# Performance work log

Hardware: AMD Instinct MI355X
Metric: run time of the kernel (lower is better)

The kernel has to match this reference:

```python
import jax, jax.numpy as jnp
import numpy as np

HEADS = 16
DIM_HEAD = 64
RMS_EPS = 1.1920929e-07  # torch.finfo(float32).eps (torch RMSNorm eps=None default)
ROPE_THETA = 10000.0


def _rope(x):
    # x: [b, h, n, d]; rotary-embedding-torch style interleaved rotation
    n, d = x.shape[-2], x.shape[-1]
    inv_freq = 1.0 / (ROPE_THETA ** (jnp.arange(0, d, 2, dtype=jnp.float32) / d))
    t = jnp.arange(n, dtype=jnp.float32)
    freqs = t[:, None] * inv_freq[None, :]              # [n, d/2]
    cos = jnp.repeat(jnp.cos(freqs), 2, axis=-1)        # [n, d] interleaved
    sin = jnp.repeat(jnp.sin(freqs), 2, axis=-1)
    x1 = x[..., ::2]
    x2 = x[..., 1::2]
    rot = jnp.stack((-x2, x1), axis=-1).reshape(x.shape)  # rotate_half, interleaved pairs
    return x * cos + rot * sin


def setup_inputs() -> dict:
    key = jax.random.key(0)
    ks = jax.random.split(key, 6)
    b, n, dim = 2, 2048, 1024
    tokens = jax.random.normal(ks[0], (b, n, dim), dtype=jnp.float32)
    norm_weight = jnp.ones((dim,), dtype=jnp.float32)
    wq = jax.random.normal(ks[1], (dim, dim), dtype=jnp.float32) * 0.02
    wk = jax.random.normal(ks[2], (dim, dim), dtype=jnp.float32) * 0.02
    wv = jax.random.normal(ks[3], (dim, dim), dtype=jnp.float32) * 0.02
    wo = jax.random.normal(ks[4], (dim, dim), dtype=jnp.float32) * 0.02
    return {"tokens": tokens, "norm_weight": norm_weight, "wq": wq, "wk": wk, "wv": wv, "wo": wo}


def reference(tokens, norm_weight, wq, wk, wv, wo):
    b, n, dim = tokens.shape
    # RMSNorm (elementwise affine)
    x = tokens * jax.lax.rsqrt(jnp.mean(tokens * tokens, axis=-1, keepdims=True) + RMS_EPS)
    x = x * norm_weight
    # QKV projections (torch Linear: x @ W.T), split heads: b n (h d) -> b h n d
    def split(y):
        return y.reshape(b, n, HEADS, DIM_HEAD).transpose(0, 2, 1, 3)
    q = split(x @ wq.T) * (DIM_HEAD ** -0.5)
    k = split(x @ wk.T)
    v = split(x @ wv.T)
    # rotary embedding (no kv cache -> same positions for q and k)
    q = _rope(q)
    k = _rope(k)
    sim = jnp.einsum('bhid,bhjd->bhij', q, k)
    causal = jnp.triu(jnp.ones((n, n), dtype=bool), k=1)
    sim = jnp.where(causal, -jnp.finfo(sim.dtype).max, sim)
    attn = jax.nn.softmax(sim, axis=-1)
    out = jnp.einsum('bhij,bhjd->bhid', attn, v)
    out = out.transpose(0, 2, 1, 3).reshape(b, n, dim)  # merge heads
    return out @ wo.T
```

## Files before the change

kernel.cpp:

```cpp
#include <hip/hip_runtime.h>

typedef __bf16 bf16x8 __attribute__((ext_vector_type(8)));
typedef float f32x4 __attribute__((ext_vector_type(4)));

#define DIM 1024
#define NSEQ 2048

#define GL2LDS(g, l) __builtin_amdgcn_global_load_lds( \
    (const __attribute__((address_space(1))) void*)(g), \
    (__attribute__((address_space(3))) void*)(l), 16, 0, 0)

__global__ __launch_bounds__(256) void cvt_kernel(const float* __restrict__ s,
                                                  __bf16* __restrict__ d) {
    int i = (blockIdx.x * 256 + threadIdx.x) * 4;
    float4 f = *(const float4*)(s + i);
    union { uint2 u; __bf16 h[4]; } p;
    p.h[0] = (__bf16)f.x; p.h[1] = (__bf16)f.y;
    p.h[2] = (__bf16)f.z; p.h[3] = (__bf16)f.w;
    *(uint2*)(d + i) = p.u;
}

__global__ __launch_bounds__(256) void rmsnorm_kernel(const float* __restrict__ x,
                                                      const float* __restrict__ g,
                                                      __bf16* __restrict__ o) {
    int row = blockIdx.x;
    int t = threadIdx.x;
    float4 xv = ((const float4*)(x + (size_t)row * DIM))[t];
    float ss = xv.x*xv.x + xv.y*xv.y + xv.z*xv.z + xv.w*xv.w;
    #pragma unroll
    for (int off = 32; off; off >>= 1) ss += __shfl_xor(ss, off, 64);
    __shared__ float red[4];
    if ((t & 63) == 0) red[t >> 6] = ss;
    __syncthreads();
    ss = red[0] + red[1] + red[2] + red[3];
    float r = rsqrtf(ss * (1.0f / 1024.0f) + 1.1920929e-07f);
    float4 gv = ((const float4*)g)[t];
    union { uint2 u; __bf16 h[4]; } p;
    p.h[0] = (__bf16)(xv.x * r * gv.x);
    p.h[1] = (__bf16)(xv.y * r * gv.y);
    p.h[2] = (__bf16)(xv.z * r * gv.z);
    p.h[3] = (__bf16)(xv.w * r * gv.w);
    *(uint2*)(o + (size_t)row * DIM + t * 4) = p.u;
}

__global__ __launch_bounds__(256) void rope_kernel(__bf16* __restrict__ x) {
    int gid = blockIdx.x * 256 + threadIdx.x;
    int row = gid >> 9;
    int pr = gid & 511;
    int pos = row & (NSEQ - 1);
    int dp = pr & 31;
    float inv = __expf(-(float)dp * (9.210340371976184f / 32.0f));
    float ang = (float)pos * inv;
    float sn, cs;
    sincosf(ang, &sn, &cs);
    size_t off = (size_t)row * DIM + pr * 2;
    union { unsigned int u; __bf16 h[2]; } p;
    p.u = *(const unsigned int*)(x + off);
    float x1 = (float)p.h[0], x2 = (float)p.h[1];
    p.h[0] = (__bf16)(x1 * cs - x2 * sn);
    p.h[1] = (__bf16)(x2 * cs + x1 * sn);
    *(unsigned int*)(x + off) = p.u;
}

template <typename CT>
__device__ __forceinline__ void gemm_body(const __bf16* __restrict__ A,
                                          const __bf16* __restrict__ B,
                                          CT* __restrict__ C,
                                          int mb, int nb, int ldc, float scale,
                                          __bf16* As, __bf16* Bs) {
    int t = threadIdx.x;
    int w = t >> 6, l = t & 63;
    int wm = (w >> 1) * 64, wn = (w & 1) * 64;
    int lrow = l & 15, lq = l >> 4;
    f32x4 acc[4][4] = {};

    int srow = w * 16 + (l >> 2);
    int sc8 = (l & 3) * 8;
    const __bf16* gA = A + (size_t)(mb * 128 + srow) * 1024 + sc8;
    const __bf16* gB = B + (size_t)(nb * 128 + srow) * 1024 + sc8;
    __bf16* lA = As + (w * 64) * 8;
    __bf16* lB = Bs + (w * 64) * 8;

    for (int kt = 0; kt < 32; ++kt) {
        int k0 = kt * 32;
        GL2LDS(gA + k0, lA);
        GL2LDS(gA + k0 + (size_t)64 * 1024, lA + 256 * 8);
        GL2LDS(gB + k0, lB);
        GL2LDS(gB + k0 + (size_t)64 * 1024, lB + 256 * 8);
        __syncthreads();
        bf16x8 af[4], bfr[4];
        #pragma unroll
        for (int i = 0; i < 4; ++i)
            af[i] = *(const bf16x8*)&As[(wm + i * 16 + lrow) * 32 + lq * 8];
        #pragma unroll
        for (int i = 0; i < 4; ++i)
            bfr[i] = *(const bf16x8*)&Bs[(wn + i * 16 + lrow) * 32 + lq * 8];
        #pragma unroll
        for (int rt = 0; rt < 4; ++rt)
            #pragma unroll
            for (int ct = 0; ct < 4; ++ct)
                acc[rt][ct] = __builtin_amdgcn_mfma_f32_16x16x32_bf16(
                    af[rt], bfr[ct], acc[rt][ct], 0, 0, 0);
        __syncthreads();
    }
    #pragma unroll
    for (int rt = 0; rt < 4; ++rt)
        #pragma unroll
        for (int ct = 0; ct < 4; ++ct)
            #pragma unroll
            for (int r = 0; r < 4; ++r) {
                int row = mb * 128 + wm + rt * 16 + lq * 4 + r;
                int col = nb * 128 + wn + ct * 16 + lrow;
                C[(size_t)row * ldc + col] = (CT)(acc[rt][ct][r] * scale);
            }
}

__global__ __launch_bounds__(256) void qkv_kernel(const __bf16* __restrict__ x,
                                                  const __bf16* __restrict__ wq,
                                                  const __bf16* __restrict__ wk,
                                                  const __bf16* __restrict__ wv,
                                                  __bf16* __restrict__ qb,
                                                  __bf16* __restrict__ kb,
                                                  __bf16* __restrict__ vtb) {
    __shared__ __bf16 As[128 * 32];
    __shared__ __bf16 Bs[128 * 32];
    int bm = blockIdx.x, bn = blockIdx.y, z = blockIdx.z;
    if (z == 0)      gemm_body<__bf16>(x,  wq, qb,  bm, bn, 1024, 0.125f, As, Bs);
    else if (z == 1) gemm_body<__bf16>(x,  wk, kb,  bm, bn, 1024, 1.0f,   As, Bs);
    else             gemm_body<__bf16>(wv, x,  vtb, bn, bm, 4096, 1.0f,   As, Bs);
}

__global__ __launch_bounds__(256) void wo_kernel(const __bf16* __restrict__ A,
                                                 const __bf16* __restrict__ B,
                                                 float* __restrict__ C) {
    __shared__ __bf16 As[128 * 32];
    __shared__ __bf16 Bs[128 * 32];
    gemm_body<float>(A, B, C, blockIdx.x, blockIdx.y, 1024, 1.0f, As, Bs);
}

__global__ __launch_bounds__(256, 4) void attn_kernel(const __bf16* __restrict__ q,
                                                      const __bf16* __restrict__ kk,
                                                      const __bf16* __restrict__ vt,
                                                      __bf16* __restrict__ o) {
    int blk = blockIdx.x;
    int qt = 31 - (blk & 31);
    int h = (blk >> 5) & 15;
    int b = blk >> 9;
    int rowbase = b * NSEQ;
    int t = threadIdx.x;
    int w = t >> 6, l = t & 63;
    int lrow = l & 15, lq = l >> 4;

    __shared__ __bf16 Kt[64 * 72];
    __shared__ __bf16 Vs[64 * 72];
    __shared__ __bf16 Ps[4 * 16 * 72];
    __bf16* pw = &Ps[w * 16 * 72];

    const __bf16* kbase = kk + (size_t)rowbase * DIM + h * 64;
    const __bf16* vbase = vt + (size_t)(h * 64) * 4096 + b * 2048;

    int row0 = t >> 3;
    int c8 = (t & 7) * 8;

    const __bf16* qp = q + (size_t)(rowbase + qt * 64 + w * 16 + lrow) * DIM + h * 64;
    bf16x8 qb0 = *(const bf16x8*)(qp + lq * 8);
    bf16x8 qb1 = *(const bf16x8*)(qp + 32 + lq * 8);

    f32x4 oacc[4] = {};
    float m_r = -1e30f, l_r = 0.0f;

    uint4 kr0, kr1, vr0, vr1;
    kr0 = *(const uint4*)(kbase + (size_t)row0 * DIM + c8);
    kr1 = *(const uint4*)(kbase + (size_t)(row0 + 32) * DIM + c8);
    vr0 = *(const uint4*)(vbase + (size_t)row0 * 4096 + c8);
    vr1 = *(const uint4*)(vbase + (size_t)(row0 + 32) * 4096 + c8);
    *(uint4*)&Kt[row0 * 72 + c8] = kr0;
    *(uint4*)&Kt[(row0 + 32) * 72 + c8] = kr1;
    *(uint4*)&Vs[row0 * 72 + c8] = vr0;
    *(uint4*)&Vs[(row0 + 32) * 72 + c8] = vr1;
    __syncthreads();

    for (int jt = 0; jt <= qt; ++jt) {
        if (jt < qt) {
            int j0 = (jt + 1) * 64;
            kr0 = *(const uint4*)(kbase + (size_t)(j0 + row0) * DIM + c8);
            kr1 = *(const uint4*)(kbase + (size_t)(j0 + row0 + 32) * DIM + c8);
            vr0 = *(const uint4*)(vbase + (size_t)row0 * 4096 + j0 + c8);
            vr1 = *(const uint4*)(vbase + (size_t)(row0 + 32) * 4096 + j0 + c8);
        }

        f32x4 st[4];
        #pragma unroll
        for (int ct = 0; ct < 4; ++ct) {
            f32x4 z = {};
            bf16x8 ka0 = *(const bf16x8*)&Kt[(ct * 16 + lrow) * 72 + lq * 8];
            bf16x8 ka1 = *(const bf16x8*)&Kt[(ct * 16 + lrow) * 72 + 32 + lq * 8];
            z = __builtin_amdgcn_mfma_f32_16x16x32_bf16(ka0, qb0, z, 0, 0, 0);
            z = __builtin_amdgcn_mfma_f32_16x16x32_bf16(ka1, qb1, z, 0, 0, 0);
            st[ct] = z;
        }
        if (jt == qt) {
            int qr = w * 16 + lrow;
            #pragma unroll
            for (int ct = 0; ct < 4; ++ct)
                #pragma unroll
                for (int r = 0; r < 4; ++r)
                    if (ct * 16 + lq * 4 + r > qr) st[ct][r] = -3.0e38f;
        }
        float mx = st[0][0];
        #pragma unroll
        for (int ct = 0; ct < 4; ++ct)
            #pragma unroll
            for (int r = 0; r < 4; ++r) mx = fmaxf(mx, st[ct][r]);
        mx = fmaxf(mx, __shfl_xor(mx, 16, 64));
        mx = fmaxf(mx, __shfl_xor(mx, 32, 64));
        float mnew = fmaxf(m_r, mx);
        float alpha = __expf(m_r - mnew);
        float ps = 0.0f;
        #pragma unroll
        for (int ct = 0; ct < 4; ++ct)
            #pragma unroll
            for (int r = 0; r < 4; ++r) {
                float p = __expf(st[ct][r] - mnew);
                st[ct][r] = p;
                ps += p;
            }
        ps += __shfl_xor(ps, 16, 64);
        ps += __shfl_xor(ps, 32, 64);
        l_r = l_r * alpha + ps;
        m_r = mnew;

        #pragma unroll
        for (int ct = 0; ct < 4; ++ct) {
            union { uint2 u; __bf16 h4[4]; } pk;
            #pragma unroll
            for (int r = 0; r < 4; ++r) pk.h4[r] = (__bf16)st[ct][r];
            *(uint2*)&pw[lrow * 72 + ct * 16 + lq * 4] = pk.u;
        }
        #pragma unroll
        for (int ct = 0; ct < 4; ++ct)
            #pragma unroll
            for (int r = 0; r < 4; ++r) oacc[ct][r] *= alpha;
        bf16x8 pb0 = *(const bf16x8*)&pw[lrow * 72 + lq * 8];
        bf16x8 pb1 = *(const bf16x8*)&pw[lrow * 72 + 32 + lq * 8];
        #pragma unroll
        for (int ct = 0; ct < 4; ++ct) {
            bf16x8 va0 = *(const bf16x8*)&Vs[(ct * 16 + lrow) * 72 + lq * 8];
            bf16x8 va1 = *(const bf16x8*)&Vs[(ct * 16 + lrow) * 72 + 32 + lq * 8];
            oacc[ct] = __builtin_amdgcn_mfma_f32_16x16x32_bf16(va0, pb0, oacc[ct], 0, 0, 0);
            oacc[ct] = __builtin_amdgcn_mfma_f32_16x16x32_bf16(va1, pb1, oacc[ct], 0, 0, 0);
        }
        __syncthreads();
        if (jt < qt) {
            *(uint4*)&Kt[row0 * 72 + c8] = kr0;
            *(uint4*)&Kt[(row0 + 32) * 72 + c8] = kr1;
            *(uint4*)&Vs[row0 * 72 + c8] = vr0;
            *(uint4*)&Vs[(row0 + 32) * 72 + c8] = vr1;
        }
        __syncthreads();
    }
    float rcp = 1.0f / l_r;
    const size_t orow = (size_t)(rowbase + qt * 64 + w * 16 + lrow) * DIM + h * 64;
    #pragma unroll
    for (int ct = 0; ct < 4; ++ct) {
        union { uint2 u; __bf16 h4[4]; } pk;
        #pragma unroll
        for (int r = 0; r < 4; ++r) pk.h4[r] = (__bf16)(oacc[ct][r] * rcp);
        *(uint2*)(o + orow + ct * 16 + lq * 4) = pk.u;
    }
}

extern "C" void kernel_launch(void* const* d_in, const int* in_sizes, int n_in,
                              void* d_out, int out_size, void* d_ws, size_t ws_size,
                              hipStream_t stream) {
    const float* tokens = (const float*)d_in[0];
    const float* gamma  = (const float*)d_in[1];
    const float* wq = (const float*)d_in[2];
    const float* wk = (const float*)d_in[3];
    const float* wv = (const float*)d_in[4];
    const float* wo = (const float*)d_in[5];

    __bf16* ws  = (__bf16*)d_ws;
    __bf16* x   = ws;
    __bf16* qb  = x   + (size_t)4096 * 1024;
    __bf16* kb  = qb  + (size_t)4096 * 1024;
    __bf16* vtb = kb  + (size_t)4096 * 1024;
    __bf16* ao  = x;
    __bf16* wob = qb;
    float*  out = (float*)d_out;

    __bf16* wqb = (__bf16*)d_out;
    __bf16* wkb = wqb + (size_t)1024 * 1024;
    __bf16* wvb = wkb + (size_t)1024 * 1024;

    cvt_kernel<<<1024, 256, 0, stream>>>(wq, wqb);
    cvt_kernel<<<1024, 256, 0, stream>>>(wk, wkb);
    cvt_kernel<<<1024, 256, 0, stream>>>(wv, wvb);

    rmsnorm_kernel<<<4096, 256, 0, stream>>>(tokens, gamma, x);

    qkv_kernel<<<dim3(32, 8, 3), 256, 0, stream>>>(x, wqb, wkb, wvb, qb, kb, vtb);

    rope_kernel<<<8192, 256, 0, stream>>>(qb);
    rope_kernel<<<8192, 256, 0, stream>>>(kb);

    attn_kernel<<<1024, 256, 0, stream>>>(qb, kb, vtb, ao);

    cvt_kernel<<<1024, 256, 0, stream>>>(wo, wob);

    wo_kernel<<<dim3(32, 8), 256, 0, stream>>>(ao, wob, out);
}
```

Measured before the change: 224.6 us.

## Enlarge attention Q tile to 128 rows and map blocks per XCD

Each attention block now processes 128 query rows (32 per wave, as two 16-row groups) instead of 64, so every K/V tile loaded into LDS feeds twice as many MFMAs and global K/V traffic is halved. Block IDs are remapped so that blocks for the same batch-head land on the same XCD, which should improve L2 reuse of K/V. Waves whose rows lie entirely before the current KV tile skip compute on the diagonal tiles. The grid halves to 512 blocks and launch bounds drop to 3 waves per SIMD, trading occupancy and parallelism for reuse, with more register pressure.

```diff
diff --git a/kernel.cpp b/kernel.cpp
--- a/kernel.cpp
+++ b/kernel.cpp
@@ -138,14 +138,18 @@
     gemm_body<float>(A, B, C, blockIdx.x, blockIdx.y, 1024, 1.0f, As, Bs);
 }
 
-__global__ __launch_bounds__(256, 4) void attn_kernel(const __bf16* __restrict__ q,
+__global__ __launch_bounds__(256, 3) void attn_kernel(const __bf16* __restrict__ q,
                                                       const __bf16* __restrict__ kk,
                                                       const __bf16* __restrict__ vt,
                                                       __bf16* __restrict__ o) {
-    int blk = blockIdx.x;
-    int qt = 31 - (blk & 31);
-    int h = (blk >> 5) & 15;
-    int b = blk >> 9;
+    int id = blockIdx.x;
+    int xcd = id & 7;
+    int slot = id >> 3;
+    int qt = 15 - (slot >> 2);
+    int bh = xcd * 4 + (slot & 3);
+    int h = bh & 15;
+    int b = bh >> 4;
+    int Q0 = qt * 128;
     int rowbase = b * NSEQ;
     int t = threadIdx.x;
     int w = t >> 6, l = t & 63;
@@ -153,8 +157,8 @@
 
     __shared__ __bf16 Kt[64 * 72];
     __shared__ __bf16 Vs[64 * 72];
-    __shared__ __bf16 Ps[4 * 16 * 72];
-    __bf16* pw = &Ps[w * 16 * 72];
+    __shared__ __bf16 Ps[4 * 32 * 72];
+    __bf16* pw = &Ps[w * 32 * 72];
 
     const __bf16* kbase = kk + (size_t)rowbase * DIM + h * 64;
     const __bf16* vbase = vt + (size_t)(h * 64) * 4096 + b * 2048;
@@ -162,12 +166,14 @@
     int row0 = t >> 3;
     int c8 = (t & 7) * 8;
 
-    const __bf16* qp = q + (size_t)(rowbase + qt * 64 + w * 16 + lrow) * DIM + h * 64;
-    bf16x8 qb0 = *(const bf16x8*)(qp + lq * 8);
-    bf16x8 qb1 = *(const bf16x8*)(qp + 32 + lq * 8);
-
-    f32x4 oacc[4] = {};
-    float m_r = -1e30f, l_r = 0.0f;
+    const __bf16* qp0 = q + (size_t)(rowbase + Q0 + w * 32 + lrow) * DIM + h * 64;
+    bf16x8 qb00 = *(const bf16x8*)(qp0 + lq * 8);
+    bf16x8 qb01 = *(const bf16x8*)(qp0 + 32 + lq * 8);
+    bf16x8 qb10 = *(const bf16x8*)(qp0 + 16 * DIM + lq * 8);
+    bf16x8 qb11 = *(const bf16x8*)(qp0 + 16 * DIM + 32 + lq * 8);
+
+    f32x4 oacc[2][4] = {};
+    float m_r[2] = {-1e30f, -1e30f}, l_r[2] = {0.0f, 0.0f};
 
     uint4 kr0, kr1, vr0, vr1;
     kr0 = *(const uint4*)(kbase + (size_t)row0 * DIM + c8);
@@ -180,78 +186,94 @@
     *(uint4*)&Vs[(row0 + 32) * 72 + c8] = vr1;
     __syncthreads();
 
-    for (int jt = 0; jt <= qt; ++jt) {
-        if (jt < qt) {
-            int j0 = (jt + 1) * 64;
-            kr0 = *(const uint4*)(kbase + (size_t)(j0 + row0) * DIM + c8);
-            kr1 = *(const uint4*)(kbase + (size_t)(j0 + row0 + 32) * DIM + c8);
-            vr0 = *(const uint4*)(vbase + (size_t)row0 * 4096 + j0 + c8);
-            vr1 = *(const uint4*)(vbase + (size_t)(row0 + 32) * 4096 + j0 + c8);
+    int T = 2 * qt + 2;
+    for (int jt = 0; jt < T; ++jt) {
+        int j0 = jt * 64;
+        if (jt + 1 < T) {
+            int jn = j0 + 64;
+            kr0 = *(const uint4*)(kbase + (size_t)(jn + row0) * DIM + c8);
+            kr1 = *(const uint4*)(kbase + (size_t)(jn + row0 + 32) * DIM + c8);
+            vr0 = *(const uint4*)(vbase + (size_t)row0 * 4096 + jn + c8);
+            vr1 = *(const uint4*)(vbase + (size_t)(row0 + 32) * 4096 + jn + c8);
         }
-
-        f32x4 st[4];
-        #pragma unroll
-        for (int ct = 0; ct < 4; ++ct) {
-            f32x4 z = {};
-            bf16x8 ka0 = *(const bf16x8*)&Kt[(ct * 16 + lrow) * 72 + lq * 8];
-            bf16x8 ka1 = *(const bf16x8*)&Kt[(ct * 16 + lrow) * 72 + 32 + lq * 8];
-            z = __builtin_amdgcn_mfma_f32_16x16x32_bf16(ka0, qb0, z, 0, 0, 0);
-            z = __builtin_amdgcn_mfma_f32_16x16x32_bf16(ka1, qb1, z, 0, 0, 0);
-            st[ct] = z;
-        }
-        if (jt == qt) {
-            int qr = w * 16 + lrow;
-            #pragma unroll
-            for (int ct = 0; ct < 4; ++ct)
-                #pragma unroll
-                for (int r = 0; r < 4; ++r)
-                    if (ct * 16 + lq * 4 + r > qr) st[ct][r] = -3.0e38f;
-        }
-        float mx = st[0][0];
-        #pragma unroll
-        for (int ct = 0; ct < 4; ++ct)
-            #pragma unroll
-            for (int r = 0; r < 4; ++r) mx = fmaxf(mx, st[ct][r]);
-        mx = fmaxf(mx, __shfl_xor(mx, 16, 64));
-        mx = fmaxf(mx, __shfl_xor(mx, 32, 64));
-        float mnew = fmaxf(m_r, mx);
-        float alpha = __expf(m_r - mnew);
-        float ps = 0.0f;
-        #pragma unroll
-        for (int ct = 0; ct < 4; ++ct)
-            #pragma unroll
-            for (int r = 0; r < 4; ++r) {
-                float p = __expf(st[ct][r] - mnew);
-                st[ct][r] = p;
-                ps += p;
-            }
-        ps += __shfl_xor(ps, 16, 64);
-        ps += __shfl_xor(ps, 32, 64);
-        l_r = l_r * alpha + ps;
-        m_r = mnew;
-
-        #pragma unroll
-        for (int ct = 0; ct < 4; ++ct) {
-            union { uint2 u; __bf16 h4[4]; } pk;
-            #pragma unroll
-            for (int r = 0; r < 4; ++r) pk.h4[r] = (__bf16)st[ct][r];
-            *(uint2*)&pw[lrow * 72 + ct * 16 + lq * 4] = pk.u;
-        }
-        #pragma unroll
-        for (int ct = 0; ct < 4; ++ct)
-            #pragma unroll
-            for (int r = 0; r < 4; ++r) oacc[ct][r] *= alpha;
-        bf16x8 pb0 = *(const bf16x8*)&pw[lrow * 72 + lq * 8];
-        bf16x8 pb1 = *(const bf16x8*)&pw[lrow * 72 + 32 + lq * 8];
-        #pragma unroll
-        for (int ct = 0; ct < 4; ++ct) {
-            bf16x8 va0 = *(const bf16x8*)&Vs[(ct * 16 + lrow) * 72 + lq * 8];
-            bf16x8 va1 = *(const bf16x8*)&Vs[(ct * 16 + lrow) * 72 + 32 + lq * 8];
-            oacc[ct] = __builtin_amdgcn_mfma_f32_16x16x32_bf16(va0, pb0, oacc[ct], 0, 0, 0);
-            oacc[ct] = __builtin_amdgcn_mfma_f32_16x16x32_bf16(va1, pb1, oacc[ct], 0, 0, 0);
+        bool active = (j0 <= Q0 + w * 32 + 31);
+        if (active) {
+            f32x4 st[2][4];
+            #pragma unroll
+            for (int ct = 0; ct < 4; ++ct) {
+                bf16x8 ka0 = *(const bf16x8*)&Kt[(ct * 16 + lrow) * 72 + lq * 8];
+                bf16x8 ka1 = *(const bf16x8*)&Kt[(ct * 16 + lrow) * 72 + 32 + lq * 8];
+                f32x4 z0 = {}, z1 = {};
+                z0 = __builtin_amdgcn_mfma_f32_16x16x32_bf16(ka0, qb00, z0, 0, 0, 0);
+                z0 = __builtin_amdgcn_mfma_f32_16x16x32_bf16(ka1, qb01, z0, 0, 0, 0);
+                z1 = __builtin_amdgcn_mfma_f32_16x16x32_bf16(ka0, qb10, z1, 0, 0, 0);
+                z1 = __builtin_amdgcn_mfma_f32_16x16x32_bf16(ka1, qb11, z1, 0, 0, 0);
+                st[0][ct] = z0;
+                st[1][ct] = z1;
+            }
+            if (jt >= 2 * qt) {
+                #pragma unroll
+                for (int g = 0; g < 2; ++g) {
+                    int qr = Q0 + w * 32 + g * 16 + lrow;
+                    #pragma unroll
+                    for (int ct = 0; ct < 4; ++ct)
+                        #pragma unroll
+                        for (int r = 0; r < 4; ++r)
+                            if (j0 + ct * 16 + lq * 4 + r > qr) st[g][ct][r] = -3.0e38f;
+                }
+            }
+            #pragma unroll
+            for (int g = 0; g < 2; ++g) {
+                float mx = st[g][0][0];
+                #pragma unroll
+                for (int ct = 0; ct < 4; ++ct)
+                    #pragma unroll
+                    for (int r = 0; r < 4; ++r) mx = fmaxf(mx, st[g][ct][r]);
+                mx = fmaxf(mx, __shfl_xor(mx, 16, 64));
+                mx = fmaxf(mx, __shfl_xor(mx, 32, 64));
+                float mnew = fmaxf(m_r[g], mx);
+                float alpha = __expf(m_r[g] - mnew);
+                float ps = 0.0f;
+                #pragma unroll
+                for (int ct = 0; ct < 4; ++ct)
+                    #pragma unroll
+                    for (int r = 0; r < 4; ++r) {
+                        float p = __expf(st[g][ct][r] - mnew);
+                        st[g][ct][r] = p;
+                        ps += p;
+                    }
+                ps += __shfl_xor(ps, 16, 64);
+                ps += __shfl_xor(ps, 32, 64);
+                l_r[g] = l_r[g] * alpha + ps;
+                m_r[g] = mnew;
+                #pragma unroll
+                for (int ct = 0; ct < 4; ++ct) {
+                    union { uint2 u; __bf16 h4[4]; } pk;
+                    #pragma unroll
+                    for (int r = 0; r < 4; ++r) pk.h4[r] = (__bf16)st[g][ct][r];
+                    *(uint2*)&pw[(g * 16 + lrow) * 72 + ct * 16 + lq * 4] = pk.u;
+                }
+                #pragma unroll
+                for (int ct = 0; ct < 4; ++ct)
+                    #pragma unroll
+                    for (int r = 0; r < 4; ++r) oacc[g][ct][r] *= alpha;
+            }
+            bf16x8 pb00 = *(const bf16x8*)&pw[lrow * 72 + lq * 8];
+            bf16x8 pb01 = *(const bf16x8*)&pw[lrow * 72 + 32 + lq * 8];
+            bf16x8 pb10 = *(const bf16x8*)&pw[(16 + lrow) * 72 + lq * 8];
+            bf16x8 pb11 = *(const bf16x8*)&pw[(16 + lrow) * 72 + 32 + lq * 8];
+            #pragma unroll
+            for (int ct = 0; ct < 4; ++ct) {
+                bf16x8 va0 = *(const bf16x8*)&Vs[(ct * 16 + lrow) * 72 + lq * 8];
+                bf16x8 va1 = *(const bf16x8*)&Vs[(ct * 16 + lrow) * 72 + 32 + lq * 8];
+                oacc[0][ct] = __builtin_amdgcn_mfma_f32_16x16x32_bf16(va0, pb00, oacc[0][ct], 0, 0, 0);
+                oacc[0][ct] = __builtin_amdgcn_mfma_f32_16x16x32_bf16(va1, pb01, oacc[0][ct], 0, 0, 0);
+                oacc[1][ct] = __builtin_amdgcn_mfma_f32_16x16x32_bf16(va0, pb10, oacc[1][ct], 0, 0, 0);
+                oacc[1][ct] = __builtin_amdgcn_mfma_f32_16x16x32_bf16(va1, pb11, oacc[1][ct], 0, 0, 0);
+            }
         }
         __syncthreads();
-        if (jt < qt) {
+        if (jt + 1 < T) {
             *(uint4*)&Kt[row0 * 72 + c8] = kr0;
             *(uint4*)&Kt[(row0 + 32) * 72 + c8] = kr1;
             *(uint4*)&Vs[row0 * 72 + c8] = vr0;
@@ -259,14 +281,17 @@
         }
         __syncthreads();
     }
-    float rcp = 1.0f / l_r;
-    const size_t orow = (size_t)(rowbase + qt * 64 + w * 16 + lrow) * DIM + h * 64;
     #pragma unroll
-    for (int ct = 0; ct < 4; ++ct) {
-        union { uint2 u; __bf16 h4[4]; } pk;
-        #pragma unroll
-        for (int r = 0; r < 4; ++r) pk.h4[r] = (__bf16)(oacc[ct][r] * rcp);
-        *(uint2*)(o + orow + ct * 16 + lq * 4) = pk.u;
+    for (int g = 0; g < 2; ++g) {
+        float rcp = 1.0f / l_r[g];
+        const size_t orow = (size_t)(rowbase + Q0 + w * 32 + g * 16 + lrow) * DIM + h * 64;
+        #pragma unroll
+        for (int ct = 0; ct < 4; ++ct) {
+            union { uint2 u; __bf16 h4[4]; } pk;
+            #pragma unroll
+            for (int r = 0; r < 4; ++r) pk.h4[r] = (__bf16)(oacc[g][ct][r] * rcp);
+            *(uint2*)(o + orow + ct * 16 + lq * 4) = pk.u;
+        }
     }
 }
 
@@ -304,7 +329,7 @@
     rope_kernel<<<8192, 256, 0, stream>>>(qb);
     rope_kernel<<<8192, 256, 0, stream>>>(kb);
 
-    attn_kernel<<<1024, 256, 0, stream>>>(qb, kb, vtb, ao);
+    attn_kernel<<<512, 256, 0, stream>>>(qb, kb, vtb, ao);
 
     cvt_kernel<<<1024, 256, 0, stream>>>(wo, wob);
 
```

New measurement: 215.0 us. -4.3%, faster.

## Use persistent XCD-local attention scheduler, double-buffered K/V, and wider GEMM k-tiles

Applied to the files above, without the earlier changes.

The attention kernel becomes persistent: 512 blocks pull work items from per-XCD atomic counters, longest query tiles first, so load balances across the causal triangle and each XCD keeps to its own heads for L2 locality. K/V tiles are double-buffered in LDS, which removes one barrier per iteration. The GEMM body now loads 64-wide k-tiles with half as many barriers. The costs are more LDS per block, lower occupancy (launch bounds 2), and an extra init kernel whose counters live in the output buffer.

```diff
diff --git a/kernel.cpp b/kernel.cpp
--- a/kernel.cpp
+++ b/kernel.cpp
@@ -19,6 +19,8 @@
     p.h[2] = (__bf16)f.z; p.h[3] = (__bf16)f.w;
     *(uint2*)(d + i) = p.u;
 }
+
+__global__ void init_kernel(int* c) { c[threadIdx.x] = 0; }
 
 __global__ __launch_bounds__(256) void rmsnorm_kernel(const float* __restrict__ x,
                                                       const float* __restrict__ g,
@@ -74,33 +76,37 @@
     int lrow = l & 15, lq = l >> 4;
     f32x4 acc[4][4] = {};
 
-    int srow = w * 16 + (l >> 2);
-    int sc8 = (l & 3) * 8;
+    int srow = w * 32 + (l >> 3);
+    int sc8 = (l & 7) * 8;
     const __bf16* gA = A + (size_t)(mb * 128 + srow) * 1024 + sc8;
     const __bf16* gB = B + (size_t)(nb * 128 + srow) * 1024 + sc8;
-    __bf16* lA = As + (w * 64) * 8;
-    __bf16* lB = Bs + (w * 64) * 8;
-
-    for (int kt = 0; kt < 32; ++kt) {
-        int k0 = kt * 32;
-        GL2LDS(gA + k0, lA);
-        GL2LDS(gA + k0 + (size_t)64 * 1024, lA + 256 * 8);
-        GL2LDS(gB + k0, lB);
-        GL2LDS(gB + k0 + (size_t)64 * 1024, lB + 256 * 8);
+    __bf16* lA = As + (size_t)(w * 32) * 64;
+    __bf16* lB = Bs + (size_t)(w * 32) * 64;
+
+    for (int kt = 0; kt < 16; ++kt) {
+        int k0 = kt * 64;
+        #pragma unroll
+        for (int c = 0; c < 4; ++c) {
+            GL2LDS(gA + (size_t)c * 8 * 1024 + k0, lA + c * 8 * 64);
+            GL2LDS(gB + (size_t)c * 8 * 1024 + k0, lB + c * 8 * 64);
+        }
         __syncthreads();
-        bf16x8 af[4], bfr[4];
         #pragma unroll
-        for (int i = 0; i < 4; ++i)
-            af[i] = *(const bf16x8*)&As[(wm + i * 16 + lrow) * 32 + lq * 8];
-        #pragma unroll
-        for (int i = 0; i < 4; ++i)
-            bfr[i] = *(const bf16x8*)&Bs[(wn + i * 16 + lrow) * 32 + lq * 8];
-        #pragma unroll
-        for (int rt = 0; rt < 4; ++rt)
-            #pragma unroll
-            for (int ct = 0; ct < 4; ++ct)
-                acc[rt][ct] = __builtin_amdgcn_mfma_f32_16x16x32_bf16(
-                    af[rt], bfr[ct], acc[rt][ct], 0, 0, 0);
+        for (int ch = 0; ch < 2; ++ch) {
+            bf16x8 af[4], bfr[4];
+            #pragma unroll
+            for (int i = 0; i < 4; ++i)
+                af[i] = *(const bf16x8*)&As[(wm + i * 16 + lrow) * 64 + ch * 32 + lq * 8];
+            #pragma unroll
+            for (int i = 0; i < 4; ++i)
+                bfr[i] = *(const bf16x8*)&Bs[(wn + i * 16 + lrow) * 64 + ch * 32 + lq * 8];
+            #pragma unroll
+            for (int rt = 0; rt < 4; ++rt)
+                #pragma unroll
+                for (int ct = 0; ct < 4; ++ct)
+                    acc[rt][ct] = __builtin_amdgcn_mfma_f32_16x16x32_bf16(
+                        af[rt], bfr[ct], acc[rt][ct], 0, 0, 0);
+        }
         __syncthreads();
     }
     #pragma unroll
@@ -122,8 +128,8 @@
                                                   __bf16* __restrict__ qb,
                                                   __bf16* __restrict__ kb,
                                                   __bf16* __restrict__ vtb) {
-    __shared__ __bf16 As[128 * 32];
-    __shared__ __bf16 Bs[128 * 32];
+    __shared__ __bf16 As[128 * 64];
+    __shared__ __bf16 Bs[128 * 64];
     int bm = blockIdx.x, bn = blockIdx.y, z = blockIdx.z;
     if (z == 0)      gemm_body<__bf16>(x,  wq, qb,  bm, bn, 1024, 0.125f, As, Bs);
     else if (z == 1) gemm_body<__bf16>(x,  wk, kb,  bm, bn, 1024, 1.0f,   As, Bs);
@@ -133,140 +139,148 @@
 __global__ __launch_bounds__(256) void wo_kernel(const __bf16* __restrict__ A,
                                                  const __bf16* __restrict__ B,
                                                  float* __restrict__ C) {
-    __shared__ __bf16 As[128 * 32];
-    __shared__ __bf16 Bs[128 * 32];
+    __shared__ __bf16 As[128 * 64];
+    __shared__ __bf16 Bs[128 * 64];
     gemm_body<float>(A, B, C, blockIdx.x, blockIdx.y, 1024, 1.0f, As, Bs);
 }
 
-__global__ __launch_bounds__(256, 4) void attn_kernel(const __bf16* __restrict__ q,
+__global__ __launch_bounds__(256, 2) void attn_kernel(const __bf16* __restrict__ q,
                                                       const __bf16* __restrict__ kk,
                                                       const __bf16* __restrict__ vt,
-                                                      __bf16* __restrict__ o) {
-    int blk = blockIdx.x;
-    int qt = 31 - (blk & 31);
-    int h = (blk >> 5) & 15;
-    int b = blk >> 9;
-    int rowbase = b * NSEQ;
+                                                      __bf16* __restrict__ o,
+                                                      int* __restrict__ counters) {
+    int xcd = blockIdx.x & 7;
     int t = threadIdx.x;
     int w = t >> 6, l = t & 63;
     int lrow = l & 15, lq = l >> 4;
-
-    __shared__ __bf16 Kt[64 * 72];
-    __shared__ __bf16 Vs[64 * 72];
-    __shared__ __bf16 Ps[4 * 16 * 72];
-    __bf16* pw = &Ps[w * 16 * 72];
-
-    const __bf16* kbase = kk + (size_t)rowbase * DIM + h * 64;
-    const __bf16* vbase = vt + (size_t)(h * 64) * 4096 + b * 2048;
-
     int row0 = t >> 3;
     int c8 = (t & 7) * 8;
 
-    const __bf16* qp = q + (size_t)(rowbase + qt * 64 + w * 16 + lrow) * DIM + h * 64;
-    bf16x8 qb0 = *(const bf16x8*)(qp + lq * 8);
-    bf16x8 qb1 = *(const bf16x8*)(qp + 32 + lq * 8);
-
-    f32x4 oacc[4] = {};
-    float m_r = -1e30f, l_r = 0.0f;
-
-    uint4 kr0, kr1, vr0, vr1;
-    kr0 = *(const uint4*)(kbase + (size_t)row0 * DIM + c8);
-    kr1 = *(const uint4*)(kbase + (size_t)(row0 + 32) * DIM + c8);
-    vr0 = *(const uint4*)(vbase + (size_t)row0 * 4096 + c8);
-    vr1 = *(const uint4*)(vbase + (size_t)(row0 + 32) * 4096 + c8);
-    *(uint4*)&Kt[row0 * 72 + c8] = kr0;
-    *(uint4*)&Kt[(row0 + 32) * 72 + c8] = kr1;
-    *(uint4*)&Vs[row0 * 72 + c8] = vr0;
-    *(uint4*)&Vs[(row0 + 32) * 72 + c8] = vr1;
-    __syncthreads();
-
-    for (int jt = 0; jt <= qt; ++jt) {
-        if (jt < qt) {
-            int j0 = (jt + 1) * 64;
-            kr0 = *(const uint4*)(kbase + (size_t)(j0 + row0) * DIM + c8);
-            kr1 = *(const uint4*)(kbase + (size_t)(j0 + row0 + 32) * DIM + c8);
-            vr0 = *(const uint4*)(vbase + (size_t)row0 * 4096 + j0 + c8);
-            vr1 = *(const uint4*)(vbase + (size_t)(row0 + 32) * 4096 + j0 + c8);
+    __shared__ __bf16 Kt[2][64 * 72];
+    __shared__ __bf16 Vs[2][64 * 72];
+    __shared__ __bf16 Ps[4 * 16 * 72];
+    __shared__ int s_item;
+    __bf16* pw = &Ps[w * 16 * 72];
+
+    for (;;) {
+        if (t == 0) s_item = atomicAdd(&counters[xcd], 1);
+        __syncthreads();
+        int item = s_item;
+        if (item >= 128) break;
+        int qt = 31 - (item >> 2);
+        int bh = xcd * 4 + (item & 3);
+        int h = bh & 15;
+        int b = bh >> 4;
+        int rowbase = b * NSEQ;
+
+        const __bf16* kbase = kk + (size_t)rowbase * DIM + h * 64;
+        const __bf16* vbase = vt + (size_t)(h * 64) * 4096 + b * 2048;
+
+        const __bf16* qp = q + (size_t)(rowbase + qt * 64 + w * 16 + lrow) * DIM + h * 64;
+        bf16x8 qb0 = *(const bf16x8*)(qp + lq * 8);
+        bf16x8 qb1 = *(const bf16x8*)(qp + 32 + lq * 8);
+
+        f32x4 oacc[4] = {};
+        float m_r = -1e30f, l_r = 0.0f;
+
+        uint4 kr0, kr1, vr0, vr1;
+        kr0 = *(const uint4*)(kbase + (size_t)row0 * DIM + c8);
+        kr1 = *(const uint4*)(kbase + (size_t)(row0 + 32) * DIM + c8);
+        vr0 = *(const uint4*)(vbase + (size_t)row0 * 4096 + c8);
+        vr1 = *(const uint4*)(vbase + (size_t)(row0 + 32) * 4096 + c8);
+        *(uint4*)&Kt[0][row0 * 72 + c8] = kr0;
+        *(uint4*)&Kt[0][(row0 + 32) * 72 + c8] = kr1;
+        *(uint4*)&Vs[0][row0 * 72 + c8] = vr0;
+        *(uint4*)&Vs[0][(row0 + 32) * 72 + c8] = vr1;
+        __syncthreads();
+
+        for (int jt = 0; jt <= qt; ++jt) {
+            int cur = jt & 1;
+            if (jt < qt) {
+                int j0 = (jt + 1) * 64;
+                kr0 = *(const uint4*)(kbase + (size_t)(j0 + row0) * DIM + c8);
+                kr1 = *(const uint4*)(kbase + (size_t)(j0 + row0 + 32) * DIM + c8);
+                vr0 = *(const uint4*)(vbase + (size_t)row0 * 4096 + j0 + c8);
+                vr1 = *(const uint4*)(vbase + (size_t)(row0 + 32) * 4096 + j0 + c8);
+            }
+            f32x4 st[4];
+            #pragma unroll
+            for (int ct = 0; ct < 4; ++ct) {
+                f32x4 z = {};
+                bf16x8 ka0 = *(const bf16x8*)&Kt[cur][(ct * 16 + lrow) * 72 + lq * 8];
+                bf16x8 ka1 = *(const bf16x8*)&Kt[cur][(ct * 16 + lrow) * 72 + 32 + lq * 8];
+                z = __builtin_amdgcn_mfma_f32_16x16x32_bf16(ka0, qb0, z, 0, 0, 0);
+                z = __builtin_amdgcn_mfma_f32_16x16x32_bf16(ka1, qb1, z, 0, 0, 0);
+                st[ct] = z;
+            }
+            if (jt == qt) {
+                int qr = w * 16 + lrow;
+                #pragma unroll
+                for (int ct = 0; ct < 4; ++ct)
+                    #pragma unroll
+                    for (int r = 0; r < 4; ++r)
+                        if (ct * 16 + lq * 4 + r > qr) st[ct][r] = -3.0e38f;
+            }
+            float mx = st[0][0];
+            #pragma unroll
+            for (int ct = 0; ct < 4; ++ct)
+                #pragma unroll
+                for (int r = 0; r < 4; ++r) mx = fmaxf(mx, st[ct][r]);
+            mx = fmaxf(mx, __shfl_xor(mx, 16, 64));
+            mx = fmaxf(mx, __shfl_xor(mx, 32, 64));
+            float mnew = fmaxf(m_r, mx);
+            float alpha = __expf(m_r - mnew);
+            float ps = 0.0f;
+            #pragma unroll
+            for (int ct = 0; ct < 4; ++ct)
+                #pragma unroll
+                for (int r = 0; r < 4; ++r) {
+                    float p = __expf(st[ct][r] - mnew);
+                    st[ct][r] = p;
+                    ps += p;
+                }
+            ps += __shfl_xor(ps, 16, 64);
+            ps += __shfl_xor(ps, 32, 64);
+            l_r = l_r * alpha + ps;
+            m_r = mnew;
+
+            #pragma unroll
+            for (int ct = 0; ct < 4; ++ct) {
+                union { uint2 u; __bf16 h4[4]; } pk;
+                #pragma unroll
+                for (int r = 0; r < 4; ++r) pk.h4[r] = (__bf16)st[ct][r];
+                *(uint2*)&pw[lrow * 72 + ct * 16 + lq * 4] = pk.u;
+            }
+            #pragma unroll
+            for (int ct = 0; ct < 4; ++ct)
+                #pragma unroll
+                for (int r = 0; r < 4; ++r) oacc[ct][r] *= alpha;
+            bf16x8 pb0 = *(const bf16x8*)&pw[lrow * 72 + lq * 8];
+            bf16x8 pb1 = *(const bf16x8*)&pw[lrow * 72 + 32 + lq * 8];
+            #pragma unroll
+            for (int ct = 0; ct < 4; ++ct) {
+                bf16x8 va0 = *(const bf16x8*)&Vs[cur][(ct * 16 + lrow) * 72 + lq * 8];
+                bf16x8 va1 = *(const bf16x8*)&Vs[cur][(ct * 16 + lrow) * 72 + 32 + lq * 8];
+                oacc[ct] = __builtin_amdgcn_mfma_f32_16x16x32_bf16(va0, pb0, oacc[ct], 0, 0, 0);
+                oacc[ct] = __builtin_amdgcn_mfma_f32_16x16x32_bf16(va1, pb1, oacc[ct], 0, 0, 0);
+            }
+            if (jt < qt) {
+                *(uint4*)&Kt[cur ^ 1][row0 * 72 + c8] = kr0;
+                *(uint4*)&Kt[cur ^ 1][(row0 + 32) * 72 + c8] = kr1;
+                *(uint4*)&Vs[cur ^ 1][row0 * 72 + c8] = vr0;
+                *(uint4*)&Vs[cur ^ 1][(row0 + 32) * 72 + c8] = vr1;
+            }
+            __syncthreads();
         }
-
-        f32x4 st[4];
-        #pragma unroll
-        for (int ct = 0; ct < 4; ++ct) {
-            f32x4 z = {};
-            bf16x8 ka0 = *(const bf16x8*)&Kt[(ct * 16 + lrow) * 72 + lq * 8];
-            bf16x8 ka1 = *(const bf16x8*)&Kt[(ct * 16 + lrow) * 72 + 32 + lq * 8];
-            z = __builtin_amdgcn_mfma_f32_16x16x32_bf16(ka0, qb0, z, 0, 0, 0);
-            z = __builtin_amdgcn_mfma_f32_16x16x32_bf16(ka1, qb1, z, 0, 0, 0);
-            st[ct] = z;
-        }
-        if (jt == qt) {
-            int qr = w * 16 + lrow;
-            #pragma unroll
-            for (int ct = 0; ct < 4; ++ct)
-                #pragma unroll
-                for (int r = 0; r < 4; ++r)
-                    if (ct * 16 + lq * 4 + r > qr) st[ct][r] = -3.0e38f;
-        }
-        float mx = st[0][0];
-        #pragma unroll
-        for (int ct = 0; ct < 4; ++ct)
-            #pragma unroll
-            for (int r = 0; r < 4; ++r) mx = fmaxf(mx, st[ct][r]);
-        mx = fmaxf(mx, __shfl_xor(mx, 16, 64));
-        mx = fmaxf(mx, __shfl_xor(mx, 32, 64));
-        float mnew = fmaxf(m_r, mx);
-        float alpha = __expf(m_r - mnew);
-        float ps = 0.0f;
-        #pragma unroll
-        for (int ct = 0; ct < 4; ++ct)
-            #pragma unroll
-            for (int r = 0; r < 4; ++r) {
-                float p = __expf(st[ct][r] - mnew);
-                st[ct][r] = p;
-                ps += p;
-            }
-        ps += __shfl_xor(ps, 16, 64);
-        ps += __shfl_xor(ps, 32, 64);
-        l_r = l_r * alpha + ps;
-        m_r = mnew;
-
+        float rcp = 1.0f / l_r;
+        const size_t orow = (size_t)(rowbase + qt * 64 + w * 16 + lrow) * DIM + h * 64;
         #pragma unroll
         for (int ct = 0; ct < 4; ++ct) {
             union { uint2 u; __bf16 h4[4]; } pk;
             #pragma unroll
-            for (int r = 0; r < 4; ++r) pk.h4[r] = (__bf16)st[ct][r];
-            *(uint2*)&pw[lrow * 72 + ct * 16 + lq * 4] = pk.u;
+            for (int r = 0; r < 4; ++r) pk.h4[r] = (__bf16)(oacc[ct][r] * rcp);
+            *(uint2*)(o + orow + ct * 16 + lq * 4) = pk.u;
         }
-        #pragma unroll
-        for (int ct = 0; ct < 4; ++ct)
-            #pragma unroll
-            for (int r = 0; r < 4; ++r) oacc[ct][r] *= alpha;
-        bf16x8 pb0 = *(const bf16x8*)&pw[lrow * 72 + lq * 8];
-        bf16x8 pb1 = *(const bf16x8*)&pw[lrow * 72 + 32 + lq * 8];
-        #pragma unroll
-        for (int ct = 0; ct < 4; ++ct) {
-            bf16x8 va0 = *(const bf16x8*)&Vs[(ct * 16 + lrow) * 72 + lq * 8];
-            bf16x8 va1 = *(const bf16x8*)&Vs[(ct * 16 + lrow) * 72 + 32 + lq * 8];
-            oacc[ct] = __builtin_amdgcn_mfma_f32_16x16x32_bf16(va0, pb0, oacc[ct], 0, 0, 0);
-            oacc[ct] = __builtin_amdgcn_mfma_f32_16x16x32_bf16(va1, pb1, oacc[ct], 0, 0, 0);
-        }
-        __syncthreads();
-        if (jt < qt) {
-            *(uint4*)&Kt[row0 * 72 + c8] = kr0;
-            *(uint4*)&Kt[(row0 + 32) * 72 + c8] = kr1;
-            *(uint4*)&Vs[row0 * 72 + c8] = vr0;
-            *(uint4*)&Vs[(row0 + 32) * 72 + c8] = vr1;
-        }
-        __syncthreads();
-    }
-    float rcp = 1.0f / l_r;
-    const size_t orow = (size_t)(rowbase + qt * 64 + w * 16 + lrow) * DIM + h * 64;
-    #pragma unroll
-    for (int ct = 0; ct < 4; ++ct) {
-        union { uint2 u; __bf16 h4[4]; } pk;
-        #pragma unroll
-        for (int r = 0; r < 4; ++r) pk.h4[r] = (__bf16)(oacc[ct][r] * rcp);
-        *(uint2*)(o + orow + ct * 16 + lq * 4) = pk.u;
     }
 }
 
@@ -292,6 +306,7 @@
     __bf16* wqb = (__bf16*)d_out;
     __bf16* wkb = wqb + (size_t)1024 * 1024;
     __bf16* wvb = wkb + (size_t)1024 * 1024;
+    int* counters = (int*)((char*)d_out + (size_t)8 * 1024 * 1024);
 
     cvt_kernel<<<1024, 256, 0, stream>>>(wq, wqb);
     cvt_kernel<<<1024, 256, 0, stream>>>(wk, wkb);
@@ -304,7 +319,9 @@
     rope_kernel<<<8192, 256, 0, stream>>>(qb);
     rope_kernel<<<8192, 256, 0, stream>>>(kb);
 
-    attn_kernel<<<1024, 256, 0, stream>>>(qb, kb, vtb, ao);
+    init_kernel<<<1, 8, 0, stream>>>(counters);
+
+    attn_kernel<<<512, 256, 0, stream>>>(qb, kb, vtb, ao, counters);
 
     cvt_kernel<<<1024, 256, 0, stream>>>(wo, wob);
 
```

New measurement: 214.9 us. 4.3% less time.
